# Performance work log

Measured on AMD Instinct MI355X. Metric: run time of the kernel, lower is better.

The kernel has to match this reference:

```python
import jax, jax.numpy as jnp
import numpy as np

EMBED_DIM = 1024
B, S = 8, 2048


def setup_inputs() -> dict:
    key = jax.random.key(0)
    ks = jax.random.split(key, 8)
    scale = 1.0 / np.sqrt(EMBED_DIM)
    return {
        "mha_output": jax.random.normal(ks[0], (B, S, EMBED_DIM), dtype=jnp.float32),
        "gates": jax.random.uniform(ks[1], (B, S), dtype=jnp.float32),
        "Wq": jax.random.uniform(ks[2], (EMBED_DIM, EMBED_DIM), jnp.float32, -scale, scale),
        "bq": jax.random.uniform(ks[3], (EMBED_DIM,), jnp.float32, -scale, scale),
        "Wk": jax.random.uniform(ks[4], (EMBED_DIM, EMBED_DIM), jnp.float32, -scale, scale),
        "bk": jax.random.uniform(ks[5], (EMBED_DIM,), jnp.float32, -scale, scale),
        "Wv": jax.random.uniform(ks[6], (EMBED_DIM, EMBED_DIM), jnp.float32, -scale, scale),
        "bv": jax.random.uniform(ks[7], (EMBED_DIM,), jnp.float32, -scale, scale),
    }


def reference(mha_output, gates, Wq, bq, Wk, bk, Wv, bv):
    # gates: (B, S) -> (B, S, 1) for elementwise modulation
    g = gates[..., None]
    # Linear layers (torch convention: x @ W^T + b)
    Q = jnp.einsum('bsd,ed->bse', mha_output, Wq) + bq
    K = jnp.einsum('bsd,ed->bse', mha_output, Wk) + bk
    V = jnp.einsum('bsd,ed->bse', mha_output, Wv) + bv
    Q_mod = Q * g
    K_mod = K * g
    temperature = jnp.sqrt(jnp.asarray(EMBED_DIM, dtype=mha_output.dtype))
    scores = jnp.einsum('bqd,bkd->bqk', Q_mod, K_mod) / temperature  # (B, S, S)
    attn_weights = jax.nn.softmax(scores, axis=-1)
    gated_attn_output = jnp.einsum('bqk,bkd->bqd', attn_weights, V)
    return gated_attn_output, attn_weights
```

## Files before the change

### kernel.cpp

```cpp
#include <hip/hip_runtime.h>

#define SEQ  2048
#define EMB  1024
#define NBAT 8
#define NROW (NBAT*SEQ)

using u16 = unsigned short;
typedef float  f32x4  __attribute__((ext_vector_type(4)));
typedef __bf16 bf16x8 __attribute__((ext_vector_type(8)));
typedef u16    u16x8  __attribute__((ext_vector_type(8)));
typedef u16    u16x4  __attribute__((ext_vector_type(4)));

__device__ __forceinline__ u16 f2bf(float x) {
  unsigned u = __builtin_bit_cast(unsigned, x);
  return (u16)((u + 0x7fffu + ((u >> 16) & 1u)) >> 16);
}
__device__ __forceinline__ float bf2f(u16 h) {
  return __builtin_bit_cast(float, ((unsigned)h) << 16);
}

__device__ __forceinline__ f32x4 mfma16(u16x8 a, u16x8 b, f32x4 c) {
  return __builtin_amdgcn_mfma_f32_16x16x32_bf16(
      __builtin_bit_cast(bf16x8, a), __builtin_bit_cast(bf16x8, b), c, 0, 0, 0);
}

__device__ __forceinline__ void async_cp16(const u16* g, u16* l) {
  __builtin_amdgcn_global_load_lds(
      (const __attribute__((address_space(1))) void*)(g),
      (__attribute__((address_space(3))) void*)(l), 16, 0, 0);
}

__device__ __forceinline__ void gload_tile(const u16* __restrict__ g, int ld,
                                           u16* __restrict__ lds, int wid, int lane)
{
#pragma unroll
  for (int l = 0; l < 2; ++l) {
    const int r0 = wid * 32 + l * 16;
    const u16* src = g + (size_t)(r0 + (lane >> 2)) * ld + (lane & 3) * 8;
    async_cp16(src, lds + r0 * 32);
  }
}

__device__ __forceinline__ void kstep(const u16* __restrict__ sA, const u16* __restrict__ sB,
                                      int wr, int wc, int lane, f32x4 acc[4][4])
{
  const int r = lane & 15, kg = lane >> 4;
  u16x8 a[4], b[4];
#pragma unroll
  for (int i = 0; i < 4; ++i) {
    a[i] = *(const u16x8*)&sA[(wr * 64 + i * 16 + r) * 32 + kg * 8];
    b[i] = *(const u16x8*)&sB[(wc * 64 + i * 16 + r) * 32 + kg * 8];
  }
#pragma unroll
  for (int i = 0; i < 4; ++i)
#pragma unroll
    for (int j = 0; j < 4; ++j)
      acc[i][j] = mfma16(a[i], b[j], acc[i][j]);
}

#define GEMM_PIPE(Aptr, ldA, Bptr, ldB, NTv)                        \
  gload_tile((Aptr), (ldA), sA0, wid, lane);                        \
  gload_tile((Bptr), (ldB), sB0, wid, lane);                        \
  gload_tile((Aptr) + 32, (ldA), sA1, wid, lane);                   \
  gload_tile((Bptr) + 32, (ldB), sB1, wid, lane);                   \
  {                                                                 \
    u16 *pa0 = sA0, *pa1 = sA1, *pa2 = sA2;                         \
    u16 *pb0 = sB0, *pb1 = sB1, *pb2 = sB2;                         \
    for (int tt = 0; tt < (NTv) - 1; ++tt) {                        \
      asm volatile("s_waitcnt vmcnt(4)" ::: "memory");              \
      __builtin_amdgcn_s_barrier();                                 \
      __builtin_amdgcn_sched_barrier(0);                            \
      if (tt + 2 < (NTv)) {                                         \
        gload_tile((Aptr) + (tt + 2) * 32, (ldA), pa2, wid, lane);  \
        gload_tile((Bptr) + (tt + 2) * 32, (ldB), pb2, wid, lane);  \
      }                                                             \
      kstep(pa0, pb0, wr, wc, lane, acc);                           \
      u16* tmp = pa0; pa0 = pa1; pa1 = pa2; pa2 = tmp;              \
      tmp = pb0; pb0 = pb1; pb1 = pb2; pb2 = tmp;                   \
    }                                                               \
    asm volatile("s_waitcnt vmcnt(0)" ::: "memory");                \
    __builtin_amdgcn_s_barrier();                                   \
    __builtin_amdgcn_sched_barrier(0);                              \
    kstep(pa0, pb0, wr, wc, lane, acc);                             \
  }

#define DECL_LDS_PIPE()                                             \
  __shared__ alignas(16) u16 sA0[128 * 32], sA1[128 * 32], sA2[128 * 32]; \
  __shared__ alignas(16) u16 sB0[128 * 32], sB1[128 * 32], sB2[128 * 32]

__device__ __forceinline__ int xcd_swz(int bid, int nwg) {
  return (bid & 7) * (nwg >> 3) + (bid >> 3);
}

__global__ __launch_bounds__(256) void prep_kernel(
    const float* __restrict__ X,
    const float* __restrict__ Wq, const float* __restrict__ Wk, const float* __restrict__ Wv,
    u16* __restrict__ Xb, u16* __restrict__ Wb)
{
  const size_t i = ((size_t)blockIdx.x * 256 + threadIdx.x) * 4;
  const size_t nx = (size_t)NROW * EMB;
  f32x4 v;
  u16* dst;
  if (i < nx) {
    v = *(const f32x4*)(X + i);
    dst = Xb + i;
  } else {
    const size_t j = i - nx;
    const int m = (int)(j / ((size_t)EMB * EMB));
    const size_t o = j - (size_t)m * EMB * EMB;
    const float* W = (m == 0) ? Wq : (m == 1) ? Wk : Wv;
    v = *(const f32x4*)(W + o);
    dst = Wb + j;
  }
  u16x4 h;
#pragma unroll
  for (int j = 0; j < 4; ++j) h[j] = f2bf(v[j]);
  *(u16x4*)dst = h;
}

__global__ __launch_bounds__(256) void proj_kernel(
    const u16* __restrict__ Xb, const u16* __restrict__ Wb,
    const float* __restrict__ bq, const float* __restrict__ bk, const float* __restrict__ bv,
    u16* __restrict__ Qb, u16* __restrict__ Kb, u16* __restrict__ VT)
{
  DECL_LDS_PIPE();

  const int nwg = (EMB / 128) * (NROW / 128) * 3;
  int wg = xcd_swz(blockIdx.x, nwg);
  const int n0 = (wg & 7) * 128;        wg >>= 3;
  const int m0 = (wg & 127) * 128;      wg >>= 7;
  const int mat = wg;

  const int t = threadIdx.x, lane = t & 63, wid = t >> 6;
  const int wr = wid >> 1, wc = wid & 1;

  const u16* A = Xb + (size_t)m0 * EMB;
  const u16* B = Wb + (size_t)mat * EMB * EMB + (size_t)n0 * EMB;

  f32x4 acc[4][4];
#pragma unroll
  for (int i = 0; i < 4; ++i)
#pragma unroll
    for (int j = 0; j < 4; ++j)
#pragma unroll
      for (int q = 0; q < 4; ++q) acc[i][j][q] = 0.0f;

  GEMM_PIPE(A, EMB, B, EMB, EMB / 32);

  const float* bias = (mat == 0) ? bq : (mat == 1) ? bk : bv;
  const int r = lane & 15, kg = lane >> 4;
#pragma unroll
  for (int i = 0; i < 4; ++i) {
#pragma unroll
    for (int j = 0; j < 4; ++j) {
      const int c = n0 + wc * 64 + j * 16 + r;
      const float bb = bias[c];
      if (mat == 2) {
        const int bi = m0 >> 11;
        const int sbase = (m0 & (SEQ - 1)) + wr * 64 + i * 16 + kg * 4;
        u16x4 hv;
#pragma unroll
        for (int rg = 0; rg < 4; ++rg) hv[rg] = f2bf(acc[i][j][rg] + bb);
        *(u16x4*)&VT[((size_t)bi * EMB + c) * SEQ + sbase] = hv;
      } else {
        u16* D = (mat == 0) ? Qb : Kb;
#pragma unroll
        for (int rg = 0; rg < 4; ++rg) {
          const int row = m0 + wr * 64 + i * 16 + kg * 4 + rg;
          D[(size_t)row * EMB + c] = f2bf(acc[i][j][rg] + bb);
        }
      }
    }
  }
}

__global__ __launch_bounds__(256) void scores_kernel(
    const u16* __restrict__ Qb, const u16* __restrict__ Kb,
    const float* __restrict__ gates, u16* __restrict__ raw)
{
  DECL_LDS_PIPE();

  const int nwg = 16 * 16 * NBAT;
  int wg = xcd_swz(blockIdx.x, nwg);
  const int n0 = (wg & 15) * 128;       wg >>= 4;
  const int q0 = (wg & 15) * 128;       wg >>= 4;
  const int b  = wg;

  const int t = threadIdx.x, lane = t & 63, wid = t >> 6;
  const int wr = wid >> 1, wc = wid & 1;

  const u16* A = Qb + ((size_t)b * SEQ + q0) * EMB;
  const u16* B = Kb + ((size_t)b * SEQ + n0) * EMB;

  f32x4 acc[4][4];
#pragma unroll
  for (int i = 0; i < 4; ++i)
#pragma unroll
    for (int j = 0; j < 4; ++j)
#pragma unroll
      for (int q = 0; q < 4; ++q) acc[i][j][q] = 0.0f;

  GEMM_PIPE(A, EMB, B, EMB, EMB / 32);

  const float* gb = gates + (size_t)b * SEQ;
  u16* rawB = raw + ((size_t)b * SEQ + q0) * SEQ;
  const int r = lane & 15, kg = lane >> 4;

  float gkj[4];
#pragma unroll
  for (int j = 0; j < 4; ++j) gkj[j] = gb[n0 + wc * 64 + j * 16 + r] * 0.03125f;

#pragma unroll
  for (int i = 0; i < 4; ++i) {
#pragma unroll
    for (int rg = 0; rg < 4; ++rg) {
      const int qr = wr * 64 + i * 16 + kg * 4 + rg;
      const float gq = gb[q0 + qr];
#pragma unroll
      for (int j = 0; j < 4; ++j) {
        const int col = n0 + wc * 64 + j * 16 + r;
        rawB[(size_t)qr * SEQ + col] = f2bf(expf(acc[i][j][rg] * gq * gkj[j]));
      }
    }
  }
}

__global__ __launch_bounds__(256) void rownorm_kernel(
    const u16* __restrict__ raw, float* __restrict__ attn, float* __restrict__ invl)
{
  const int row = blockIdx.x;
  const int t = threadIdx.x, lane = t & 63, wid = t >> 6;
  const u16* rp = raw + (size_t)row * SEQ + t * 8;
  u16x8 h = *(const u16x8*)rp;
  float e[8];
  float s = 0.f;
#pragma unroll
  for (int j = 0; j < 8; ++j) { e[j] = bf2f(h[j]); s += e[j]; }
#pragma unroll
  for (int off = 32; off >= 1; off >>= 1) s += __shfl_xor(s, off);
  __shared__ float red[4];
  if (lane == 0) red[wid] = s;
  __syncthreads();
  s = (red[0] + red[1]) + (red[2] + red[3]);
  const float iv = 1.0f / s;
  float* ap = attn + (size_t)row * SEQ + t * 8;
  f32x4 w0, w1;
#pragma unroll
  for (int j = 0; j < 4; ++j) { w0[j] = e[j] * iv; w1[j] = e[j + 4] * iv; }
  *(f32x4*)ap       = w0;
  *(f32x4*)(ap + 4) = w1;
  if (t == 0) invl[row] = iv;
}

__global__ __launch_bounds__(256) void pv_kernel(
    const u16* __restrict__ Eb, const u16* __restrict__ VT,
    const float* __restrict__ invl, float* __restrict__ out)
{
  DECL_LDS_PIPE();

  const int nwg = 8 * 16 * NBAT;
  int wg = xcd_swz(blockIdx.x, nwg);
  const int d0 = (wg & 7) * 128;        wg >>= 3;
  const int q0 = (wg & 15) * 128;       wg >>= 4;
  const int b  = wg;

  const int t = threadIdx.x, lane = t & 63, wid = t >> 6;
  const int wr = wid >> 1, wc = wid & 1;

  const u16* A = Eb + ((size_t)b * SEQ + q0) * SEQ;
  const u16* B = VT + ((size_t)b * EMB + d0) * SEQ;

  f32x4 acc[4][4];
#pragma unroll
  for (int i = 0; i < 4; ++i)
#pragma unroll
    for (int j = 0; j < 4; ++j)
#pragma unroll
      for (int q = 0; q < 4; ++q) acc[i][j][q] = 0.0f;

  GEMM_PIPE(A, SEQ, B, SEQ, SEQ / 32);

  const int r = lane & 15, kg = lane >> 4;
#pragma unroll
  for (int i = 0; i < 4; ++i) {
#pragma unroll
    for (int rg = 0; rg < 4; ++rg) {
      const int rowl = q0 + wr * 64 + i * 16 + kg * 4 + rg;
      const float iv = invl[(size_t)b * SEQ + rowl];
#pragma unroll
      for (int j = 0; j < 4; ++j) {
        const int col = d0 + wc * 64 + j * 16 + r;
        out[((size_t)b * SEQ + rowl) * EMB + col] = acc[i][j][rg] * iv;
      }
    }
  }
}

extern "C" void kernel_launch(void* const* d_in, const int* in_sizes, int n_in,
                              void* d_out, int out_size, void* d_ws, size_t ws_size,
                              hipStream_t stream) {
  const float* X  = (const float*)d_in[0];
  const float* g  = (const float*)d_in[1];
  const float* Wq = (const float*)d_in[2];
  const float* bq = (const float*)d_in[3];
  const float* Wk = (const float*)d_in[4];
  const float* bk = (const float*)d_in[5];
  const float* Wv = (const float*)d_in[6];
  const float* bv = (const float*)d_in[7];

  float* out0 = (float*)d_out;
  float* attn = out0 + (size_t)NROW * EMB;

  const size_t rawN = (size_t)NBAT * SEQ * SEQ;
  const size_t need = rawN * 2 + (size_t)NBAT * EMB * SEQ * 2 + (size_t)NROW * 4;
  if (ws_size < need) return;
  u16* region0 = (u16*)d_ws;
  u16* Xb  = region0;
  u16* Wb  = region0 + (size_t)NROW * EMB;
  u16* raw = region0;
  u16* VT  = region0 + rawN;
  float* invl = (float*)(VT + (size_t)NBAT * EMB * SEQ);
  u16* Qb = (u16*)out0;
  u16* Kb = Qb + (size_t)NROW * EMB;

  const int prep_blocks = (int)(((size_t)NROW * EMB + (size_t)3 * EMB * EMB) / 1024);
  prep_kernel   <<<dim3(prep_blocks), 256, 0, stream>>>(X, Wq, Wk, Wv, Xb, Wb);
  proj_kernel   <<<dim3((EMB / 128) * (NROW / 128) * 3), 256, 0, stream>>>(
      Xb, Wb, bq, bk, bv, Qb, Kb, VT);
  scores_kernel <<<dim3(16 * 16 * NBAT), 256, 0, stream>>>(Qb, Kb, g, raw);
  rownorm_kernel<<<dim3(NROW), 256, 0, stream>>>(raw, attn, invl);
  pv_kernel     <<<dim3(8 * 16 * NBAT), 256, 0, stream>>>(raw, VT, invl, out0);
}
```

Baseline: 377.9 us.

## Switch GEMMs to 256x256 tiles with 8-wave phased pipeline and swizzled LDS

All three GEMM kernels (projection, scores, PV) move from 128x128 tiles with 4 waves to 256x256 tiles with 8 waves. The K loop is split into four phases per 64-wide K step, interleaving LDS reads, async global-to-LDS staging and MFMA blocks, with barriers and s_setprio around each phase. The LDS layout gets an XOR swizzle to avoid bank conflicts. The aim is more data reuse per tile and better overlap of loads with compute. The cost is fewer workgroups (256 for PV on a chip with many CUs), more accumulator registers and a larger LDS footprint, which may reduce occupancy.

```diff
diff --git a/kernel.cpp b/kernel.cpp
--- a/kernel.cpp
+++ b/kernel.cpp
@@ -30,63 +30,118 @@
       (__attribute__((address_space(3))) void*)(l), 16, 0, 0);
 }
 
-__device__ __forceinline__ void gload_tile(const u16* __restrict__ g, int ld,
+__device__ __forceinline__ void stage_half(const u16* __restrict__ g, int ld,
                                            u16* __restrict__ lds, int wid, int lane)
 {
+  const int lr = lane >> 2;
+  const int bb = (lr & 1) ^ ((lr >> 2) & 1);
+  const int row16 = (lr & ~1) | bb;
+  const int ck = (lane & 3) ^ ((lr & 2) | bb);
 #pragma unroll
   for (int l = 0; l < 2; ++l) {
     const int r0 = wid * 32 + l * 16;
-    const u16* src = g + (size_t)(r0 + (lane >> 2)) * ld + (lane & 3) * 8;
-    async_cp16(src, lds + r0 * 32);
-  }
-}
-
-__device__ __forceinline__ void kstep(const u16* __restrict__ sA, const u16* __restrict__ sB,
-                                      int wr, int wc, int lane, f32x4 acc[4][4])
-{
-  const int r = lane & 15, kg = lane >> 4;
-  u16x8 a[4], b[4];
+    async_cp16(g + (size_t)(r0 + row16) * ld + ck * 8, lds + r0 * 32);
+  }
+}
+
+__device__ __forceinline__ void ph_reads_A(const u16* __restrict__ sAh, int mg,
+                                           int wr, int r, int kg, int xr, u16x8 a[4])
+{
 #pragma unroll
   for (int i = 0; i < 4; ++i) {
-    a[i] = *(const u16x8*)&sA[(wr * 64 + i * 16 + r) * 32 + kg * 8];
-    b[i] = *(const u16x8*)&sB[(wc * 64 + i * 16 + r) * 32 + kg * 8];
-  }
+    const int row = wr * 128 + (mg * 4 + i) * 16 + r;
+    a[i] = *(const u16x8*)&sAh[(row * 32 + kg * 8) ^ xr];
+  }
+}
+__device__ __forceinline__ void ph_reads_B(const u16* __restrict__ sBh,
+                                           int wc, int r, int kg, int xr, u16x8 b[4])
+{
+#pragma unroll
+  for (int j = 0; j < 4; ++j) {
+    const int row = wc * 64 + j * 16 + r;
+    b[j] = *(const u16x8*)&sBh[(row * 32 + kg * 8) ^ xr];
+  }
+}
+
+__device__ __forceinline__ void mfma_block(const u16x8 a[4], const u16x8 b[4],
+                                           f32x4 (*accp)[4])
+{
 #pragma unroll
   for (int i = 0; i < 4; ++i)
 #pragma unroll
     for (int j = 0; j < 4; ++j)
-      acc[i][j] = mfma16(a[i], b[j], acc[i][j]);
-}
-
-#define GEMM_PIPE(Aptr, ldA, Bptr, ldB, NTv)                        \
-  gload_tile((Aptr), (ldA), sA0, wid, lane);                        \
-  gload_tile((Bptr), (ldB), sB0, wid, lane);                        \
-  gload_tile((Aptr) + 32, (ldA), sA1, wid, lane);                   \
-  gload_tile((Bptr) + 32, (ldB), sB1, wid, lane);                   \
-  {                                                                 \
-    u16 *pa0 = sA0, *pa1 = sA1, *pa2 = sA2;                         \
-    u16 *pb0 = sB0, *pb1 = sB1, *pb2 = sB2;                         \
-    for (int tt = 0; tt < (NTv) - 1; ++tt) {                        \
-      asm volatile("s_waitcnt vmcnt(4)" ::: "memory");              \
-      __builtin_amdgcn_s_barrier();                                 \
-      __builtin_amdgcn_sched_barrier(0);                            \
-      if (tt + 2 < (NTv)) {                                         \
-        gload_tile((Aptr) + (tt + 2) * 32, (ldA), pa2, wid, lane);  \
-        gload_tile((Bptr) + (tt + 2) * 32, (ldB), pb2, wid, lane);  \
-      }                                                             \
-      kstep(pa0, pb0, wr, wc, lane, acc);                           \
-      u16* tmp = pa0; pa0 = pa1; pa1 = pa2; pa2 = tmp;              \
-      tmp = pb0; pb0 = pb1; pb1 = pb2; pb2 = tmp;                   \
-    }                                                               \
-    asm volatile("s_waitcnt vmcnt(0)" ::: "memory");                \
-    __builtin_amdgcn_s_barrier();                                   \
-    __builtin_amdgcn_sched_barrier(0);                              \
-    kstep(pa0, pb0, wr, wc, lane, acc);                             \
-  }
-
-#define DECL_LDS_PIPE()                                             \
-  __shared__ alignas(16) u16 sA0[128 * 32], sA1[128 * 32], sA2[128 * 32]; \
-  __shared__ alignas(16) u16 sB0[128 * 32], sB1[128 * 32], sB2[128 * 32]
+      accp[i][j] = mfma16(a[i], b[j], accp[i][j]);
+}
+
+#define DECL_LDS_8PH()                                                       \
+  __shared__ alignas(16) u16 sAls[2][2][256 * 32];                           \
+  __shared__ alignas(16) u16 sBls[2][2][256 * 32]
+
+#define PH(READS, STAGE, WAIT, ACCBASE)                                      \
+  READS                                                                      \
+  STAGE                                                                      \
+  WAIT                                                                       \
+  __builtin_amdgcn_s_barrier();                                              \
+  asm volatile("s_waitcnt lgkmcnt(0)" ::: "memory");                         \
+  __builtin_amdgcn_sched_barrier(0);                                         \
+  __builtin_amdgcn_s_setprio(1);                                             \
+  mfma_block(a_, b_, &acc[ACCBASE]);                                         \
+  __builtin_amdgcn_s_setprio(0);                                             \
+  __builtin_amdgcn_s_barrier();
+
+#define W_NONE {}
+#define W_K1  { if (pf_) asm volatile("s_waitcnt vmcnt(4)" ::: "memory");    \
+                else     asm volatile("s_waitcnt vmcnt(0)" ::: "memory");    \
+                __builtin_amdgcn_sched_barrier(0); }
+#define W_K0N { if (pf_) { asm volatile("s_waitcnt vmcnt(4)" ::: "memory");  \
+                __builtin_amdgcn_sched_barrier(0); } }
+
+#define GEMM_8PH(Aptr, ldA, Bptr, ldB, NTv)                                  \
+  {                                                                          \
+    const int r_ = lane & 15, kg_ = lane >> 4;                               \
+    const int xr_ = (r_ & 7) << 3;                                           \
+    stage_half((Aptr),      (ldA), &sAls[0][0][0], wid, lane);               \
+    stage_half((Bptr),      (ldB), &sBls[0][0][0], wid, lane);               \
+    stage_half((Aptr) + 32, (ldA), &sAls[0][1][0], wid, lane);               \
+    stage_half((Bptr) + 32, (ldB), &sBls[0][1][0], wid, lane);               \
+    asm volatile("s_waitcnt vmcnt(4)" ::: "memory");                         \
+    __builtin_amdgcn_sched_barrier(0);                                       \
+    __builtin_amdgcn_s_barrier();                                            \
+    u16x8 a_[4], b_[4];                                                      \
+    for (int tt = 0; tt < (NTv); ++tt) {                                     \
+      const int s_ = tt & 1, s2_ = s_ ^ 1;                                   \
+      const u16* A0_ = &sAls[s_][0][0]; const u16* A1_ = &sAls[s_][1][0];    \
+      const u16* B0_ = &sBls[s_][0][0]; const u16* B1_ = &sBls[s_][1][0];    \
+      const bool pf_ = (tt + 1 < (NTv));                                     \
+      PH({ ph_reads_A(A0_, 0, wr, r_, kg_, xr_, a_);                         \
+           ph_reads_B(B0_, wc, r_, kg_, xr_, b_); },                         \
+         { if (pf_) stage_half((Aptr) + (tt + 1) * 64, (ldA),                \
+                               &sAls[s2_][0][0], wid, lane); },              \
+         W_NONE, 0)                                                          \
+      PH({ ph_reads_A(A0_, 1, wr, r_, kg_, xr_, a_); },                      \
+         { if (pf_) stage_half((Bptr) + (tt + 1) * 64, (ldB),                \
+                               &sBls[s2_][0][0], wid, lane); },              \
+         W_K1, 4)                                                            \
+      PH({ ph_reads_A(A1_, 0, wr, r_, kg_, xr_, a_);                         \
+           ph_reads_B(B1_, wc, r_, kg_, xr_, b_); },                         \
+         { if (pf_) stage_half((Aptr) + (tt + 1) * 64 + 32, (ldA),           \
+                               &sAls[s2_][1][0], wid, lane); },              \
+         W_NONE, 0)                                                          \
+      PH({ ph_reads_A(A1_, 1, wr, r_, kg_, xr_, a_); },                      \
+         { if (pf_) stage_half((Bptr) + (tt + 1) * 64 + 32, (ldB),           \
+                               &sBls[s2_][1][0], wid, lane); },              \
+         W_K0N, 4)                                                           \
+    }                                                                        \
+  }
+
+#define DECL_ACC()                                                           \
+  f32x4 acc[8][4];                                                           \
+  _Pragma("unroll")                                                          \
+  for (int i = 0; i < 8; ++i)                                                \
+    _Pragma("unroll")                                                        \
+    for (int j = 0; j < 4; ++j)                                              \
+      _Pragma("unroll")                                                      \
+      for (int q = 0; q < 4; ++q) acc[i][j][q] = 0.0f
 
 __device__ __forceinline__ int xcd_swz(int bid, int nwg) {
   return (bid & 7) * (nwg >> 3) + (bid >> 3);
@@ -118,46 +173,38 @@
   *(u16x4*)dst = h;
 }
 
-__global__ __launch_bounds__(256) void proj_kernel(
+__global__ __launch_bounds__(512, 2) void proj_kernel(
     const u16* __restrict__ Xb, const u16* __restrict__ Wb,
     const float* __restrict__ bq, const float* __restrict__ bk, const float* __restrict__ bv,
     u16* __restrict__ Qb, u16* __restrict__ Kb, u16* __restrict__ VT)
 {
-  DECL_LDS_PIPE();
-
-  const int nwg = (EMB / 128) * (NROW / 128) * 3;
+  DECL_LDS_8PH();
+  const int nwg = 4 * 64 * 3;
   int wg = xcd_swz(blockIdx.x, nwg);
-  const int n0 = (wg & 7) * 128;        wg >>= 3;
-  const int m0 = (wg & 127) * 128;      wg >>= 7;
+  const int n0 = (wg & 3) * 256;        wg >>= 2;
+  const int m0 = (wg & 63) * 256;       wg >>= 6;
   const int mat = wg;
 
   const int t = threadIdx.x, lane = t & 63, wid = t >> 6;
-  const int wr = wid >> 1, wc = wid & 1;
+  const int wr = wid >> 2, wc = wid & 3;
 
   const u16* A = Xb + (size_t)m0 * EMB;
   const u16* B = Wb + (size_t)mat * EMB * EMB + (size_t)n0 * EMB;
 
-  f32x4 acc[4][4];
-#pragma unroll
-  for (int i = 0; i < 4; ++i)
-#pragma unroll
-    for (int j = 0; j < 4; ++j)
-#pragma unroll
-      for (int q = 0; q < 4; ++q) acc[i][j][q] = 0.0f;
-
-  GEMM_PIPE(A, EMB, B, EMB, EMB / 32);
+  DECL_ACC();
+  GEMM_8PH(A, EMB, B, EMB, EMB / 64);
 
   const float* bias = (mat == 0) ? bq : (mat == 1) ? bk : bv;
   const int r = lane & 15, kg = lane >> 4;
 #pragma unroll
-  for (int i = 0; i < 4; ++i) {
+  for (int i = 0; i < 8; ++i) {
 #pragma unroll
     for (int j = 0; j < 4; ++j) {
       const int c = n0 + wc * 64 + j * 16 + r;
       const float bb = bias[c];
       if (mat == 2) {
         const int bi = m0 >> 11;
-        const int sbase = (m0 & (SEQ - 1)) + wr * 64 + i * 16 + kg * 4;
+        const int sbase = (m0 & (SEQ - 1)) + wr * 128 + i * 16 + kg * 4;
         u16x4 hv;
 #pragma unroll
         for (int rg = 0; rg < 4; ++rg) hv[rg] = f2bf(acc[i][j][rg] + bb);
@@ -166,7 +213,7 @@
         u16* D = (mat == 0) ? Qb : Kb;
 #pragma unroll
         for (int rg = 0; rg < 4; ++rg) {
-          const int row = m0 + wr * 64 + i * 16 + kg * 4 + rg;
+          const int row = m0 + wr * 128 + i * 16 + kg * 4 + rg;
           D[(size_t)row * EMB + c] = f2bf(acc[i][j][rg] + bb);
         }
       }
@@ -174,33 +221,25 @@
   }
 }
 
-__global__ __launch_bounds__(256) void scores_kernel(
+__global__ __launch_bounds__(512, 2) void scores_kernel(
     const u16* __restrict__ Qb, const u16* __restrict__ Kb,
     const float* __restrict__ gates, u16* __restrict__ raw)
 {
-  DECL_LDS_PIPE();
-
-  const int nwg = 16 * 16 * NBAT;
+  DECL_LDS_8PH();
+  const int nwg = 8 * 8 * NBAT;
   int wg = xcd_swz(blockIdx.x, nwg);
-  const int n0 = (wg & 15) * 128;       wg >>= 4;
-  const int q0 = (wg & 15) * 128;       wg >>= 4;
+  const int n0 = (wg & 7) * 256;        wg >>= 3;
+  const int q0 = (wg & 7) * 256;        wg >>= 3;
   const int b  = wg;
 
   const int t = threadIdx.x, lane = t & 63, wid = t >> 6;
-  const int wr = wid >> 1, wc = wid & 1;
+  const int wr = wid >> 2, wc = wid & 3;
 
   const u16* A = Qb + ((size_t)b * SEQ + q0) * EMB;
   const u16* B = Kb + ((size_t)b * SEQ + n0) * EMB;
 
-  f32x4 acc[4][4];
-#pragma unroll
-  for (int i = 0; i < 4; ++i)
-#pragma unroll
-    for (int j = 0; j < 4; ++j)
-#pragma unroll
-      for (int q = 0; q < 4; ++q) acc[i][j][q] = 0.0f;
-
-  GEMM_PIPE(A, EMB, B, EMB, EMB / 32);
+  DECL_ACC();
+  GEMM_8PH(A, EMB, B, EMB, EMB / 64);
 
   const float* gb = gates + (size_t)b * SEQ;
   u16* rawB = raw + ((size_t)b * SEQ + q0) * SEQ;
@@ -211,10 +250,10 @@
   for (int j = 0; j < 4; ++j) gkj[j] = gb[n0 + wc * 64 + j * 16 + r] * 0.03125f;
 
 #pragma unroll
-  for (int i = 0; i < 4; ++i) {
+  for (int i = 0; i < 8; ++i) {
 #pragma unroll
     for (int rg = 0; rg < 4; ++rg) {
-      const int qr = wr * 64 + i * 16 + kg * 4 + rg;
+      const int qr = wr * 128 + i * 16 + kg * 4 + rg;
       const float gq = gb[q0 + qr];
 #pragma unroll
       for (int j = 0; j < 4; ++j) {
@@ -252,40 +291,32 @@
   if (t == 0) invl[row] = iv;
 }
 
-__global__ __launch_bounds__(256) void pv_kernel(
+__global__ __launch_bounds__(512, 2) void pv_kernel(
     const u16* __restrict__ Eb, const u16* __restrict__ VT,
     const float* __restrict__ invl, float* __restrict__ out)
 {
-  DECL_LDS_PIPE();
-
-  const int nwg = 8 * 16 * NBAT;
+  DECL_LDS_8PH();
+  const int nwg = 4 * 8 * NBAT;
   int wg = xcd_swz(blockIdx.x, nwg);
-  const int d0 = (wg & 7) * 128;        wg >>= 3;
-  const int q0 = (wg & 15) * 128;       wg >>= 4;
+  const int d0 = (wg & 3) * 256;        wg >>= 2;
+  const int q0 = (wg & 7) * 256;        wg >>= 3;
   const int b  = wg;
 
   const int t = threadIdx.x, lane = t & 63, wid = t >> 6;
-  const int wr = wid >> 1, wc = wid & 1;
+  const int wr = wid >> 2, wc = wid & 3;
 
   const u16* A = Eb + ((size_t)b * SEQ + q0) * SEQ;
   const u16* B = VT + ((size_t)b * EMB + d0) * SEQ;
 
-  f32x4 acc[4][4];
-#pragma unroll
-  for (int i = 0; i < 4; ++i)
-#pragma unroll
-    for (int j = 0; j < 4; ++j)
-#pragma unroll
-      for (int q = 0; q < 4; ++q) acc[i][j][q] = 0.0f;
-
-  GEMM_PIPE(A, SEQ, B, SEQ, SEQ / 32);
+  DECL_ACC();
+  GEMM_8PH(A, SEQ, B, SEQ, SEQ / 64);
 
   const int r = lane & 15, kg = lane >> 4;
 #pragma unroll
-  for (int i = 0; i < 4; ++i) {
+  for (int i = 0; i < 8; ++i) {
 #pragma unroll
     for (int rg = 0; rg < 4; ++rg) {
-      const int rowl = q0 + wr * 64 + i * 16 + kg * 4 + rg;
+      const int rowl = q0 + wr * 128 + i * 16 + kg * 4 + rg;
       const float iv = invl[(size_t)b * SEQ + rowl];
 #pragma unroll
       for (int j = 0; j < 4; ++j) {
@@ -325,9 +356,8 @@
 
   const int prep_blocks = (int)(((size_t)NROW * EMB + (size_t)3 * EMB * EMB) / 1024);
   prep_kernel   <<<dim3(prep_blocks), 256, 0, stream>>>(X, Wq, Wk, Wv, Xb, Wb);
-  proj_kernel   <<<dim3((EMB / 128) * (NROW / 128) * 3), 256, 0, stream>>>(
-      Xb, Wb, bq, bk, bv, Qb, Kb, VT);
-  scores_kernel <<<dim3(16 * 16 * NBAT), 256, 0, stream>>>(Qb, Kb, g, raw);
+  proj_kernel   <<<dim3(768), 512, 0, stream>>>(Xb, Wb, bq, bk, bv, Qb, Kb, VT);
+  scores_kernel <<<dim3(512), 512, 0, stream>>>(Qb, Kb, g, raw);
   rownorm_kernel<<<dim3(NROW), 256, 0, stream>>>(raw, attn, invl);
-  pv_kernel     <<<dim3(8 * 16 * NBAT), 256, 0, stream>>>(raw, VT, invl, out0);
-}
+  pv_kernel     <<<dim3(256), 512, 0, stream>>>(raw, VT, invl, out0);
+}
```

After: 372.8 us. Within noise of the previous version (-1.4%).
